# Optimization experiments

Measured on AMD Instinct MI355X. Metric: run time of the kernel, lower is better.

## Reference

```python
import jax, jax.numpy as jnp
import numpy as np

N_NODES = 100000


def gcn_conv(x, src, dst, norm, W, b, n_nodes):
    # x: [N, Din]; src/dst: [E'] (with self-loops); norm: [E']
    h = x @ W  # [N, Dout] dense transform first (PyG GCNConv order)
    msgs = h[src] * norm[:, None]  # gather + degree scaling, [E', Dout]
    out = jax.ops.segment_sum(msgs, dst, num_segments=n_nodes)  # scatter-add
    return out + b


def setup_inputs() -> dict:
    key = jax.random.key(0)
    k_x, k_e, k_w1, k_w2 = jax.random.split(key, 4)
    input_dim, hidden_dim = 256, 128
    n_edges = 1600000
    x = jax.random.normal(k_x, (N_NODES, input_dim), dtype=jnp.float32)
    edge_index = jax.random.randint(k_e, (2, n_edges), 0, N_NODES, dtype=jnp.int64)
    # Glorot-style init for conv weights, zeros bias (PyG defaults)
    s1 = (6.0 / (input_dim + hidden_dim)) ** 0.5
    s2 = (6.0 / (hidden_dim + hidden_dim)) ** 0.5
    W1 = jax.random.uniform(k_w1, (input_dim, hidden_dim), jnp.float32, -s1, s1)
    W2 = jax.random.uniform(k_w2, (hidden_dim, hidden_dim), jnp.float32, -s2, s2)
    b1 = jnp.zeros((hidden_dim,), jnp.float32)
    b2 = jnp.zeros((hidden_dim,), jnp.float32)
    return {"x": x, "edge_index": edge_index, "W1": W1, "b1": b1, "W2": W2, "b2": b2}


def reference(x, edge_index, W1, b1, W2, b2):
    n = x.shape[0]
    loops = jnp.arange(n, dtype=edge_index.dtype)
    src = jnp.concatenate([edge_index[0], loops])  # add self-loops
    dst = jnp.concatenate([edge_index[1], loops])
    # symmetric normalization deg^-1/2 (in-degree including self-loops)
    deg = jax.ops.segment_sum(jnp.ones_like(dst, dtype=x.dtype), dst, num_segments=n)
    dinv = jax.lax.rsqrt(deg)
    norm = dinv[src] * dinv[dst]
    # layer 1: GCNConv -> ReLU (dropout is identity in eval mode)
    h = jax.nn.relu(gcn_conv(x, src, dst, norm, W1, b1, n))
    # layer 2
    h = jax.nn.relu(gcn_conv(h, src, dst, norm, W2, b2, n))
    return h
```

## Files before the change

### kernel.cpp

```cpp
#include <hip/hip_runtime.h>
#include <hip/hip_bf16.h>


#define DIN 256
#define DH 128
#define BKT_SHIFT 9
#define BKT_SZ 512

typedef __attribute__((ext_vector_type(8))) short short8;
typedef __attribute__((ext_vector_type(4))) float f32x4;

__device__ __forceinline__ unsigned short f2bf(float f) {
    union { float f; unsigned int i; } c;
    c.f = f;
    unsigned int r = c.i + 0x7FFFu + ((c.i >> 16) & 1u);
    return (unsigned short)(r >> 16);
}
__device__ __forceinline__ float bf_lo(unsigned int u) {
    union { unsigned int i; float f; } c;
    c.i = u << 16;
    return c.f;
}
__device__ __forceinline__ float bf_hi(unsigned int u) {
    union { unsigned int i; float f; } c;
    c.i = u & 0xFFFF0000u;
    return c.f;
}

__global__ void count_k(const int* __restrict__ dst, int* __restrict__ cnt, int e) {
    int i = blockIdx.x * 256 + threadIdx.x;
    if (i < e) atomicAdd(&cnt[dst[i]], 1);
}

__global__ void dinv_k(const int* __restrict__ cnt, float* __restrict__ dinv, int n) {
    int i = blockIdx.x * 256 + threadIdx.x;
    if (i < n) dinv[i] = 1.0f / sqrtf((float)(cnt[i] + 1));
}

__global__ void block_sum_k(const int* __restrict__ cnt, int* __restrict__ bsum, int n) {
    __shared__ int s[256];
    int t = threadIdx.x;
    int i = blockIdx.x * 256 + t;
    s[t] = (i < n) ? cnt[i] : 0;
    __syncthreads();
    for (int off = 128; off > 0; off >>= 1) {
        if (t < off) s[t] += s[t + off];
        __syncthreads();
    }
    if (t == 0) bsum[blockIdx.x] = s[0];
}

__global__ void scan_bsum_k(int* __restrict__ bsum, int nb) {
    __shared__ int s[512];
    int t = threadIdx.x;
    s[t] = (t < nb) ? bsum[t] : 0;
    __syncthreads();
    for (int off = 1; off < 512; off <<= 1) {
        int x = (t >= off) ? s[t - off] : 0;
        __syncthreads();
        s[t] += x;
        __syncthreads();
    }
    if (t < nb) bsum[t] = (t == 0) ? 0 : s[t - 1];
}

__global__ void scan_write_k(const int* __restrict__ cnt, const int* __restrict__ bsum,
                             int* __restrict__ rowptr, int n) {
    __shared__ int s[256];
    int t = threadIdx.x;
    int i = blockIdx.x * 256 + t;
    int c = (i < n) ? cnt[i] : 0;
    s[t] = c;
    __syncthreads();
    for (int off = 1; off < 256; off <<= 1) {
        int x = (t >= off) ? s[t - off] : 0;
        __syncthreads();
        s[t] += x;
        __syncthreads();
    }
    int excl = s[t] - c + bsum[blockIdx.x];
    if (i < n) {
        rowptr[i] = excl;
        if (i == n - 1) rowptr[n] = excl + c;
    }
}

__global__ void init_bcur_k(const int* __restrict__ rowptr, int* __restrict__ bcur, int nbkt) {
    int b = threadIdx.x;
    if (b < nbkt) bcur[b] = rowptr[b << BKT_SHIFT];
}

__global__ void wt_k(const float* __restrict__ W, unsigned short* __restrict__ Wt, int K) {
    int i = blockIdx.x * 256 + threadIdx.x;
    if (i < K * 128) {
        int k = i >> 7, n = i & 127;
        Wt[(size_t)n * K + k] = f2bf(W[i]);
    }
}

__global__ __launch_bounds__(256) void bucket_k(const int* __restrict__ src,
                                                const int* __restrict__ dst,
                                                const float* __restrict__ dinv,
                                                int* __restrict__ bcur,
                                                int2* __restrict__ tmp, int e, int n) {
    __shared__ int hist[256];
    __shared__ int rstart[256];
    int nbkt = (n + BKT_SZ - 1) >> BKT_SHIFT;
    int t = threadIdx.x;
    int nb = gridDim.x;
    int chunk = (e + nb - 1) / nb;
    int beg = blockIdx.x * chunk, end = min(e, beg + chunk);

    hist[t] = 0;
    __syncthreads();
    for (int i = beg + t; i < end; i += 256) atomicAdd(&hist[dst[i] >> BKT_SHIFT], 1);
    __syncthreads();
    int h = hist[t];
    if (t < nbkt && h > 0) rstart[t] = atomicAdd(&bcur[t], h);
    __syncthreads();
    hist[t] = 0;
    __syncthreads();
    for (int i = beg + t; i < end; i += 256) {
        int d = dst[i];
        int b = d >> BKT_SHIFT;
        int o = atomicAdd(&hist[b], 1);
        int s = src[i];
        float w = dinv[s] * dinv[d];
        tmp[rstart[b] + o] = make_int2(s | ((d & (BKT_SZ - 1)) << 20), __float_as_int(w));
    }
}

__global__ __launch_bounds__(1024) void scatter2_k(const int2* __restrict__ tmp,
                                                   const int* __restrict__ rowptr,
                                                   int2* __restrict__ einfo, int n) {
    __shared__ int cur[BKT_SZ];
    int b = blockIdx.x;
    int t = threadIdx.x;
    int lo = b << BKT_SHIFT;
    int hi = min(n, lo + BKT_SZ);
    int nn = hi - lo;
    if (t < nn) cur[t] = rowptr[lo + t];
    __syncthreads();
    int beg = rowptr[lo], end = rowptr[hi];
    for (int i = beg + t; i < end; i += 1024) {
        int2 r = tmp[i];
        int dlow = (r.x >> 20) & (BKT_SZ - 1);
        int pos = atomicAdd(&cur[dlow], 1);
        einfo[pos] = make_int2(r.x & 0xFFFFF, r.y);
    }
}

template <bool A_BF16>
__global__ __launch_bounds__(256) void gemm_mfma(const void* __restrict__ Av,
                                                 const unsigned short* __restrict__ Wt,
                                                 unsigned short* __restrict__ Hb,
                                                 int M, int K) {
    __shared__ unsigned short Bt[16384];
    const int t = threadIdx.x;
    const int w = t >> 6;
    const int lane = t & 63;
    const int l15 = lane & 15;
    const int quad = lane >> 4;
    const int row0 = blockIdx.x * 128 + w * 32;

    const float* Af = (const float*)Av;
    const unsigned short* Ab = (const unsigned short*)Av;

    f32x4 acc[2][8];
#pragma unroll
    for (int rt = 0; rt < 2; ++rt)
#pragma unroll
        for (int ct = 0; ct < 8; ++ct)
#pragma unroll
            for (int j = 0; j < 4; ++j) acc[rt][ct][j] = 0.0f;

    for (int kc = 0; kc < K; kc += 128) {
        if (kc) __syncthreads();
#pragma unroll
        for (int i = 0; i < 8; ++i) {
            int fg = w * 8 + i;
            int ks = fg >> 3, ct = fg & 7;
            int nn = ct * 16 + l15;
            int gk = ks * 32 + quad * 8;
            *(short8*)&Bt[fg * 512 + lane * 8] =
                *(const short8*)(Wt + (size_t)nn * K + kc + gk);
        }
        __syncthreads();
#pragma unroll
        for (int ks = 0; ks < 4; ++ks) {
            int kk = ks * 32 + quad * 8;
            short8 af[2];
#pragma unroll
            for (int rt = 0; rt < 2; ++rt) {
                int row = row0 + rt * 16 + l15;
                if (row < M) {
                    if (A_BF16) {
                        af[rt] = *(const short8*)(Ab + (size_t)row * K + kc + kk);
                    } else {
                        const float* p = Af + (size_t)row * K + kc + kk;
                        float4 x0 = *(const float4*)p;
                        float4 x1 = *(const float4*)(p + 4);
                        af[rt][0] = (short)f2bf(x0.x);
                        af[rt][1] = (short)f2bf(x0.y);
                        af[rt][2] = (short)f2bf(x0.z);
                        af[rt][3] = (short)f2bf(x0.w);
                        af[rt][4] = (short)f2bf(x1.x);
                        af[rt][5] = (short)f2bf(x1.y);
                        af[rt][6] = (short)f2bf(x1.z);
                        af[rt][7] = (short)f2bf(x1.w);
                    }
                } else {
#pragma unroll
                    for (int j = 0; j < 8; ++j) af[rt][j] = 0;
                }
            }
#pragma unroll
            for (int ct = 0; ct < 8; ++ct) {
                short8 bfr = *(const short8*)&Bt[(ks * 8 + ct) * 512 + lane * 8];
                acc[0][ct] = __builtin_amdgcn_mfma_f32_16x16x32_bf16(af[0], bfr, acc[0][ct], 0, 0, 0);
                acc[1][ct] = __builtin_amdgcn_mfma_f32_16x16x32_bf16(af[1], bfr, acc[1][ct], 0, 0, 0);
            }
        }
    }
#pragma unroll
    for (int rt = 0; rt < 2; ++rt)
#pragma unroll
        for (int r = 0; r < 4; ++r) {
            int row = row0 + rt * 16 + quad * 4 + r;
            if (row < M) {
                unsigned short* o = Hb + (size_t)row * 128 + l15;
#pragma unroll
                for (int ct = 0; ct < 8; ++ct) o[ct * 16] = f2bf(acc[rt][ct][r]);
            }
        }
}

template <bool OUT_BF16>
__global__ __launch_bounds__(256) void agg_k(const unsigned short* __restrict__ Hb,
                                             const int* __restrict__ rowptr,
                                             const int2* __restrict__ einfo,
                                             const float* __restrict__ dinv,
                                             const float* __restrict__ bias,
                                             void* __restrict__ out, int n) {
    int v = blockIdx.x * 4 + (threadIdx.x >> 6);
    int lane = threadIdx.x & 63;
    if (v >= n) return;
    int l = lane & 31, half = lane >> 5;
    const uint2* __restrict__ H = (const uint2*)Hb;
    float a0 = 0.f, a1 = 0.f, a2 = 0.f, a3 = 0.f;
    if (half == 0) {
        float dv = dinv[v];
        float self = dv * dv;
        uint2 hv = H[(size_t)v * 32 + l];
        a0 = self * bf_lo(hv.x); a1 = self * bf_hi(hv.x);
        a2 = self * bf_lo(hv.y); a3 = self * bf_hi(hv.y);
    }
    int end = rowptr[v + 1];
    int i = rowptr[v] + half;
    for (; i + 6 < end; i += 8) {
        int2 e0 = einfo[i], e1 = einfo[i + 2], e2 = einfo[i + 4], e3 = einfo[i + 6];
        uint2 v0 = H[(size_t)e0.x * 32 + l];
        uint2 v1 = H[(size_t)e1.x * 32 + l];
        uint2 v2 = H[(size_t)e2.x * 32 + l];
        uint2 v3 = H[(size_t)e3.x * 32 + l];
        float w0 = __int_as_float(e0.y), w1 = __int_as_float(e1.y);
        float w2 = __int_as_float(e2.y), w3 = __int_as_float(e3.y);
        a0 = fmaf(w0, bf_lo(v0.x), a0); a1 = fmaf(w0, bf_hi(v0.x), a1);
        a2 = fmaf(w0, bf_lo(v0.y), a2); a3 = fmaf(w0, bf_hi(v0.y), a3);
        a0 = fmaf(w1, bf_lo(v1.x), a0); a1 = fmaf(w1, bf_hi(v1.x), a1);
        a2 = fmaf(w1, bf_lo(v1.y), a2); a3 = fmaf(w1, bf_hi(v1.y), a3);
        a0 = fmaf(w2, bf_lo(v2.x), a0); a1 = fmaf(w2, bf_hi(v2.x), a1);
        a2 = fmaf(w2, bf_lo(v2.y), a2); a3 = fmaf(w2, bf_hi(v2.y), a3);
        a0 = fmaf(w3, bf_lo(v3.x), a0); a1 = fmaf(w3, bf_hi(v3.x), a1);
        a2 = fmaf(w3, bf_lo(v3.y), a2); a3 = fmaf(w3, bf_hi(v3.y), a3);
    }
    for (; i < end; i += 2) {
        int2 e = einfo[i];
        uint2 vv = H[(size_t)e.x * 32 + l];
        float w = __int_as_float(e.y);
        a0 = fmaf(w, bf_lo(vv.x), a0); a1 = fmaf(w, bf_hi(vv.x), a1);
        a2 = fmaf(w, bf_lo(vv.y), a2); a3 = fmaf(w, bf_hi(vv.y), a3);
    }
    a0 += __shfl_xor(a0, 32);
    a1 += __shfl_xor(a1, 32);
    a2 += __shfl_xor(a2, 32);
    a3 += __shfl_xor(a3, 32);
    if (half == 0) {
        float4 bb = ((const float4*)bias)[l];
        float o0 = fmaxf(a0 + bb.x, 0.f);
        float o1 = fmaxf(a1 + bb.y, 0.f);
        float o2 = fmaxf(a2 + bb.z, 0.f);
        float o3 = fmaxf(a3 + bb.w, 0.f);
        if (OUT_BF16) {
            unsigned int p0 = (unsigned int)f2bf(o0) | ((unsigned int)f2bf(o1) << 16);
            unsigned int p1 = (unsigned int)f2bf(o2) | ((unsigned int)f2bf(o3) << 16);
            ((uint2*)out)[(size_t)v * 32 + l] = make_uint2(p0, p1);
        } else {
            ((float4*)out)[(size_t)v * 32 + l] = make_float4(o0, o1, o2, o3);
        }
    }
}

static inline size_t align_up(size_t x, size_t a) { return (x + a - 1) & ~(a - 1); }

extern "C" void kernel_launch(void* const* d_in, const int* in_sizes, int n_in,
                              void* d_out, int out_size, void* d_ws, size_t ws_size,
                              hipStream_t stream) {
    const float* x  = (const float*)d_in[0];
    const int*   ei = (const int*)d_in[1];
    const float* W1 = (const float*)d_in[2];
    const float* b1 = (const float*)d_in[3];
    const float* W2 = (const float*)d_in[4];
    const float* b2 = (const float*)d_in[5];

    const int N = in_sizes[0] / DIN;
    const int E = in_sizes[1] / 2;
    const int* src = ei;
    const int* dst = ei + E;
    const int NBKT = (N + BKT_SZ - 1) >> BKT_SHIFT;

    char* base = (char*)d_ws;
    size_t off = 0;
    int* cnt = (int*)(base + off);          off = align_up(off + (size_t)N * 4, 256);
    int* rowptr = (int*)(base + off);       off = align_up(off + (size_t)(N + 1) * 4, 256);
    float* dinv = (float*)(base + off);     off = align_up(off + (size_t)N * 4, 256);
    int* bsum = (int*)(base + off);         off = align_up(off + 512 * 4, 256);
    int* bcur = (int*)(base + off);         off = align_up(off + 256 * 4, 256);
    int2* tmp = (int2*)(base + off);        off = align_up(off + (size_t)E * 8, 256);
    int2* einfo = (int2*)(base + off);      off = align_up(off + (size_t)E * 8, 256);
    unsigned short* Wt1 = (unsigned short*)(base + off); off = align_up(off + (size_t)128 * 256 * 2, 256);
    unsigned short* Wt2 = (unsigned short*)(base + off); off = align_up(off + (size_t)128 * 128 * 2, 256);
    unsigned short* hb  = (unsigned short*)(base + off); off = align_up(off + (size_t)N * 128 * 2, 256);
    unsigned short* a1b = (unsigned short*)(base + off); off = align_up(off + (size_t)N * 128 * 2, 256);

    float* out = (float*)d_out;
    const int NB = (N + 255) / 256;

    hipMemsetAsync(cnt, 0, (size_t)N * sizeof(int), stream);
    count_k<<<(E + 255) / 256, 256, 0, stream>>>(dst, cnt, E);
    dinv_k<<<NB, 256, 0, stream>>>(cnt, dinv, N);
    block_sum_k<<<NB, 256, 0, stream>>>(cnt, bsum, N);
    scan_bsum_k<<<1, 512, 0, stream>>>(bsum, NB);
    scan_write_k<<<NB, 256, 0, stream>>>(cnt, bsum, rowptr, N);
    init_bcur_k<<<1, 256, 0, stream>>>(rowptr, bcur, NBKT);
    wt_k<<<(256 * 128 + 255) / 256, 256, 0, stream>>>(W1, Wt1, 256);
    wt_k<<<(128 * 128 + 255) / 256, 256, 0, stream>>>(W2, Wt2, 128);

    bucket_k<<<512, 256, 0, stream>>>(src, dst, dinv, bcur, tmp, E, N);
    scatter2_k<<<NBKT, 1024, 0, stream>>>(tmp, rowptr, einfo, N);

    const int GB = (N + 127) / 128;
    gemm_mfma<false><<<GB, 256, 0, stream>>>(x, Wt1, hb, N, DIN);
    agg_k<true><<<(N + 3) / 4, 256, 0, stream>>>(hb, rowptr, einfo, dinv, b1, a1b, N);
    gemm_mfma<true><<<GB, 256, 0, stream>>>(a1b, Wt2, hb, N, DH);
    agg_k<false><<<(N + 3) / 4, 256, 0, stream>>>(hb, rowptr, einfo, dinv, b2, out, N);
}
```

Before: 498.3 us.

## Fold GCN normalization into GEMM epilogue and fuse CSR build into fewer kernels

The degree-count and multi-kernel scan pipeline is replaced by a fused prep kernel that buckets edges into fixed-capacity per-bucket regions and also converts the weights. A single-block bucket scan follows, and the per-bucket scatter now computes the degrees, dinv and rowptr itself. The symmetric normalization is refactored so the GEMM epilogue scales each row by dinv[src] and aggregation applies dinv[dst] once at the end. Edge records therefore shrink from 8 to 4 bytes and the per-edge multiply disappears. Aggregation uses nontemporal loads and stores. The fixed CAP of 10240 records per bucket assumes a roughly uniform in-degree distribution and would overflow on skewed graphs.

```diff
diff --git a/kernel.cpp b/kernel.cpp
--- a/kernel.cpp
+++ b/kernel.cpp
@@ -6,9 +6,12 @@
 #define DH 128
 #define BKT_SHIFT 9
 #define BKT_SZ 512
+#define NBKT_MAX 256
+#define CAP 10240
 
 typedef __attribute__((ext_vector_type(8))) short short8;
 typedef __attribute__((ext_vector_type(4))) float f32x4;
+typedef __attribute__((ext_vector_type(2))) unsigned int uint2e;
 
 __device__ __forceinline__ unsigned short f2bf(float f) {
     union { float f; unsigned int i; } c;
@@ -27,96 +30,41 @@
     return c.f;
 }
 
-__global__ void count_k(const int* __restrict__ dst, int* __restrict__ cnt, int e) {
-    int i = blockIdx.x * 256 + threadIdx.x;
-    if (i < e) atomicAdd(&cnt[dst[i]], 1);
-}
-
-__global__ void dinv_k(const int* __restrict__ cnt, float* __restrict__ dinv, int n) {
-    int i = blockIdx.x * 256 + threadIdx.x;
-    if (i < n) dinv[i] = 1.0f / sqrtf((float)(cnt[i] + 1));
-}
-
-__global__ void block_sum_k(const int* __restrict__ cnt, int* __restrict__ bsum, int n) {
-    __shared__ int s[256];
+__global__ __launch_bounds__(256) void prep_k(const int* __restrict__ src,
+                                              const int* __restrict__ dst,
+                                              int* __restrict__ bcnt,
+                                              int* __restrict__ tmp, int e, int n,
+                                              int NBB,
+                                              const float* __restrict__ W1,
+                                              const float* __restrict__ W2,
+                                              unsigned short* __restrict__ Wt1,
+                                              unsigned short* __restrict__ Wt2) {
+    int bx = blockIdx.x;
     int t = threadIdx.x;
-    int i = blockIdx.x * 256 + t;
-    s[t] = (i < n) ? cnt[i] : 0;
-    __syncthreads();
-    for (int off = 128; off > 0; off >>= 1) {
-        if (t < off) s[t] += s[t + off];
-        __syncthreads();
-    }
-    if (t == 0) bsum[blockIdx.x] = s[0];
-}
-
-__global__ void scan_bsum_k(int* __restrict__ bsum, int nb) {
-    __shared__ int s[512];
-    int t = threadIdx.x;
-    s[t] = (t < nb) ? bsum[t] : 0;
-    __syncthreads();
-    for (int off = 1; off < 512; off <<= 1) {
-        int x = (t >= off) ? s[t - off] : 0;
-        __syncthreads();
-        s[t] += x;
-        __syncthreads();
-    }
-    if (t < nb) bsum[t] = (t == 0) ? 0 : s[t - 1];
-}
-
-__global__ void scan_write_k(const int* __restrict__ cnt, const int* __restrict__ bsum,
-                             int* __restrict__ rowptr, int n) {
-    __shared__ int s[256];
-    int t = threadIdx.x;
-    int i = blockIdx.x * 256 + t;
-    int c = (i < n) ? cnt[i] : 0;
-    s[t] = c;
-    __syncthreads();
-    for (int off = 1; off < 256; off <<= 1) {
-        int x = (t >= off) ? s[t - off] : 0;
-        __syncthreads();
-        s[t] += x;
-        __syncthreads();
-    }
-    int excl = s[t] - c + bsum[blockIdx.x];
-    if (i < n) {
-        rowptr[i] = excl;
-        if (i == n - 1) rowptr[n] = excl + c;
-    }
-}
-
-__global__ void init_bcur_k(const int* __restrict__ rowptr, int* __restrict__ bcur, int nbkt) {
-    int b = threadIdx.x;
-    if (b < nbkt) bcur[b] = rowptr[b << BKT_SHIFT];
-}
-
-__global__ void wt_k(const float* __restrict__ W, unsigned short* __restrict__ Wt, int K) {
-    int i = blockIdx.x * 256 + threadIdx.x;
-    if (i < K * 128) {
-        int k = i >> 7, n = i & 127;
-        Wt[(size_t)n * K + k] = f2bf(W[i]);
-    }
-}
-
-__global__ __launch_bounds__(256) void bucket_k(const int* __restrict__ src,
-                                                const int* __restrict__ dst,
-                                                const float* __restrict__ dinv,
-                                                int* __restrict__ bcur,
-                                                int2* __restrict__ tmp, int e, int n) {
-    __shared__ int hist[256];
-    __shared__ int rstart[256];
+    if (bx >= NBB) {
+        int i = (bx - NBB) * 256 + t;
+        if (i < 256 * 128) {
+            int k = i >> 7, nn = i & 127;
+            Wt1[(size_t)nn * 256 + k] = f2bf(W1[i]);
+        } else if (i < 256 * 128 + 128 * 128) {
+            int j = i - 256 * 128;
+            int k = j >> 7, nn = j & 127;
+            Wt2[(size_t)nn * 128 + k] = f2bf(W2[j]);
+        }
+        return;
+    }
+    __shared__ int hist[NBKT_MAX];
+    __shared__ int rstart[NBKT_MAX];
     int nbkt = (n + BKT_SZ - 1) >> BKT_SHIFT;
-    int t = threadIdx.x;
-    int nb = gridDim.x;
-    int chunk = (e + nb - 1) / nb;
-    int beg = blockIdx.x * chunk, end = min(e, beg + chunk);
+    int chunk = (e + NBB - 1) / NBB;
+    int beg = bx * chunk, end = min(e, beg + chunk);
 
     hist[t] = 0;
     __syncthreads();
     for (int i = beg + t; i < end; i += 256) atomicAdd(&hist[dst[i] >> BKT_SHIFT], 1);
     __syncthreads();
     int h = hist[t];
-    if (t < nbkt && h > 0) rstart[t] = atomicAdd(&bcur[t], h);
+    if (t < nbkt && h > 0) rstart[t] = atomicAdd(&bcnt[t], h);
     __syncthreads();
     hist[t] = 0;
     __syncthreads();
@@ -124,35 +72,77 @@
         int d = dst[i];
         int b = d >> BKT_SHIFT;
         int o = atomicAdd(&hist[b], 1);
-        int s = src[i];
-        float w = dinv[s] * dinv[d];
-        tmp[rstart[b] + o] = make_int2(s | ((d & (BKT_SZ - 1)) << 20), __float_as_int(w));
-    }
-}
-
-__global__ __launch_bounds__(1024) void scatter2_k(const int2* __restrict__ tmp,
-                                                   const int* __restrict__ rowptr,
-                                                   int2* __restrict__ einfo, int n) {
+        tmp[(size_t)b * CAP + rstart[b] + o] = src[i] | ((d & (BKT_SZ - 1)) << 20);
+    }
+}
+
+__global__ void scan196_k(const int* __restrict__ bcnt, int* __restrict__ base,
+                          int* __restrict__ rowptr, int nbkt, int n) {
+    __shared__ int s[256];
+    int t = threadIdx.x;
+    s[t] = (t < nbkt) ? bcnt[t] : 0;
+    __syncthreads();
+    for (int off = 1; off < 256; off <<= 1) {
+        int x = (t >= off) ? s[t - off] : 0;
+        __syncthreads();
+        s[t] += x;
+        __syncthreads();
+    }
+    base[t] = (t == 0) ? 0 : s[t - 1];
+    if (t == nbkt - 1) {
+        base[nbkt] = s[t];
+        rowptr[n] = s[t];
+    }
+}
+
+__global__ __launch_bounds__(1024) void scatter2_k(const int* __restrict__ tmp,
+                                                   const int* __restrict__ bcnt,
+                                                   const int* __restrict__ base,
+                                                   float* __restrict__ dinv,
+                                                   int* __restrict__ rowptr,
+                                                   int* __restrict__ einfo, int n) {
+    __shared__ int hist[BKT_SZ];
+    __shared__ int scn[BKT_SZ];
     __shared__ int cur[BKT_SZ];
     int b = blockIdx.x;
     int t = threadIdx.x;
     int lo = b << BKT_SHIFT;
-    int hi = min(n, lo + BKT_SZ);
-    int nn = hi - lo;
-    if (t < nn) cur[t] = rowptr[lo + t];
-    __syncthreads();
-    int beg = rowptr[lo], end = rowptr[hi];
-    for (int i = beg + t; i < end; i += 1024) {
-        int2 r = tmp[i];
-        int dlow = (r.x >> 20) & (BKT_SZ - 1);
+    int nn = min(n - lo, BKT_SZ);
+    int cnt = bcnt[b];
+    int bas = base[b];
+    const int* rec = tmp + (size_t)b * CAP;
+    if (t < BKT_SZ) hist[t] = 0;
+    __syncthreads();
+    for (int i = t; i < cnt; i += 1024) atomicAdd(&hist[(rec[i] >> 20) & (BKT_SZ - 1)], 1);
+    __syncthreads();
+    if (t < BKT_SZ) scn[t] = hist[t];
+    __syncthreads();
+    for (int off = 1; off < BKT_SZ; off <<= 1) {
+        int x = 0;
+        if (t < BKT_SZ && t >= off) x = scn[t - off];
+        __syncthreads();
+        if (t < BKT_SZ) scn[t] += x;
+        __syncthreads();
+    }
+    if (t < nn) {
+        int excl = bas + scn[t] - hist[t];
+        dinv[lo + t] = 1.0f / sqrtf((float)(hist[t] + 1));
+        rowptr[lo + t] = excl;
+        cur[t] = excl;
+    }
+    __syncthreads();
+    for (int i = t; i < cnt; i += 1024) {
+        int r = rec[i];
+        int dlow = (r >> 20) & (BKT_SZ - 1);
         int pos = atomicAdd(&cur[dlow], 1);
-        einfo[pos] = make_int2(r.x & 0xFFFFF, r.y);
+        einfo[pos] = r & 0xFFFFF;
     }
 }
 
 template <bool A_BF16>
 __global__ __launch_bounds__(256) void gemm_mfma(const void* __restrict__ Av,
                                                  const unsigned short* __restrict__ Wt,
+                                                 const float* __restrict__ dinv,
                                                  unsigned short* __restrict__ Hb,
                                                  int M, int K) {
     __shared__ unsigned short Bt[16384];
@@ -228,9 +218,10 @@
         for (int r = 0; r < 4; ++r) {
             int row = row0 + rt * 16 + quad * 4 + r;
             if (row < M) {
+                float dv = dinv[row];
                 unsigned short* o = Hb + (size_t)row * 128 + l15;
 #pragma unroll
-                for (int ct = 0; ct < 8; ++ct) o[ct * 16] = f2bf(acc[rt][ct][r]);
+                for (int ct = 0; ct < 8; ++ct) o[ct * 16] = f2bf(dv * acc[rt][ct][r]);
             }
         }
 }
@@ -238,7 +229,7 @@
 template <bool OUT_BF16>
 __global__ __launch_bounds__(256) void agg_k(const unsigned short* __restrict__ Hb,
                                              const int* __restrict__ rowptr,
-                                             const int2* __restrict__ einfo,
+                                             const int* __restrict__ einfo,
                                              const float* __restrict__ dinv,
                                              const float* __restrict__ bias,
                                              void* __restrict__ out, int n) {
@@ -249,54 +240,50 @@
     const uint2* __restrict__ H = (const uint2*)Hb;
     float a0 = 0.f, a1 = 0.f, a2 = 0.f, a3 = 0.f;
     if (half == 0) {
-        float dv = dinv[v];
-        float self = dv * dv;
         uint2 hv = H[(size_t)v * 32 + l];
-        a0 = self * bf_lo(hv.x); a1 = self * bf_hi(hv.x);
-        a2 = self * bf_lo(hv.y); a3 = self * bf_hi(hv.y);
+        a0 = bf_lo(hv.x); a1 = bf_hi(hv.x);
+        a2 = bf_lo(hv.y); a3 = bf_hi(hv.y);
     }
     int end = rowptr[v + 1];
     int i = rowptr[v] + half;
     for (; i + 6 < end; i += 8) {
-        int2 e0 = einfo[i], e1 = einfo[i + 2], e2 = einfo[i + 4], e3 = einfo[i + 6];
-        uint2 v0 = H[(size_t)e0.x * 32 + l];
-        uint2 v1 = H[(size_t)e1.x * 32 + l];
-        uint2 v2 = H[(size_t)e2.x * 32 + l];
-        uint2 v3 = H[(size_t)e3.x * 32 + l];
-        float w0 = __int_as_float(e0.y), w1 = __int_as_float(e1.y);
-        float w2 = __int_as_float(e2.y), w3 = __int_as_float(e3.y);
-        a0 = fmaf(w0, bf_lo(v0.x), a0); a1 = fmaf(w0, bf_hi(v0.x), a1);
-        a2 = fmaf(w0, bf_lo(v0.y), a2); a3 = fmaf(w0, bf_hi(v0.y), a3);
-        a0 = fmaf(w1, bf_lo(v1.x), a0); a1 = fmaf(w1, bf_hi(v1.x), a1);
-        a2 = fmaf(w1, bf_lo(v1.y), a2); a3 = fmaf(w1, bf_hi(v1.y), a3);
-        a0 = fmaf(w2, bf_lo(v2.x), a0); a1 = fmaf(w2, bf_hi(v2.x), a1);
-        a2 = fmaf(w2, bf_lo(v2.y), a2); a3 = fmaf(w2, bf_hi(v2.y), a3);
-        a0 = fmaf(w3, bf_lo(v3.x), a0); a1 = fmaf(w3, bf_hi(v3.x), a1);
-        a2 = fmaf(w3, bf_lo(v3.y), a2); a3 = fmaf(w3, bf_hi(v3.y), a3);
+        int s0 = __builtin_nontemporal_load(&einfo[i]);
+        int s1 = __builtin_nontemporal_load(&einfo[i + 2]);
+        int s2 = __builtin_nontemporal_load(&einfo[i + 4]);
+        int s3 = __builtin_nontemporal_load(&einfo[i + 6]);
+        uint2 v0 = H[(size_t)s0 * 32 + l];
+        uint2 v1 = H[(size_t)s1 * 32 + l];
+        uint2 v2 = H[(size_t)s2 * 32 + l];
+        uint2 v3 = H[(size_t)s3 * 32 + l];
+        a0 += bf_lo(v0.x); a1 += bf_hi(v0.x); a2 += bf_lo(v0.y); a3 += bf_hi(v0.y);
+        a0 += bf_lo(v1.x); a1 += bf_hi(v1.x); a2 += bf_lo(v1.y); a3 += bf_hi(v1.y);
+        a0 += bf_lo(v2.x); a1 += bf_hi(v2.x); a2 += bf_lo(v2.y); a3 += bf_hi(v2.y);
+        a0 += bf_lo(v3.x); a1 += bf_hi(v3.x); a2 += bf_lo(v3.y); a3 += bf_hi(v3.y);
     }
     for (; i < end; i += 2) {
-        int2 e = einfo[i];
-        uint2 vv = H[(size_t)e.x * 32 + l];
-        float w = __int_as_float(e.y);
-        a0 = fmaf(w, bf_lo(vv.x), a0); a1 = fmaf(w, bf_hi(vv.x), a1);
-        a2 = fmaf(w, bf_lo(vv.y), a2); a3 = fmaf(w, bf_hi(vv.y), a3);
+        int s = __builtin_nontemporal_load(&einfo[i]);
+        uint2 vv = H[(size_t)s * 32 + l];
+        a0 += bf_lo(vv.x); a1 += bf_hi(vv.x); a2 += bf_lo(vv.y); a3 += bf_hi(vv.y);
     }
     a0 += __shfl_xor(a0, 32);
     a1 += __shfl_xor(a1, 32);
     a2 += __shfl_xor(a2, 32);
     a3 += __shfl_xor(a3, 32);
     if (half == 0) {
+        float dv = dinv[v];
         float4 bb = ((const float4*)bias)[l];
-        float o0 = fmaxf(a0 + bb.x, 0.f);
-        float o1 = fmaxf(a1 + bb.y, 0.f);
-        float o2 = fmaxf(a2 + bb.z, 0.f);
-        float o3 = fmaxf(a3 + bb.w, 0.f);
+        float o0 = fmaxf(fmaf(dv, a0, bb.x), 0.f);
+        float o1 = fmaxf(fmaf(dv, a1, bb.y), 0.f);
+        float o2 = fmaxf(fmaf(dv, a2, bb.z), 0.f);
+        float o3 = fmaxf(fmaf(dv, a3, bb.w), 0.f);
         if (OUT_BF16) {
-            unsigned int p0 = (unsigned int)f2bf(o0) | ((unsigned int)f2bf(o1) << 16);
-            unsigned int p1 = (unsigned int)f2bf(o2) | ((unsigned int)f2bf(o3) << 16);
-            ((uint2*)out)[(size_t)v * 32 + l] = make_uint2(p0, p1);
+            uint2e p;
+            p.x = (unsigned int)f2bf(o0) | ((unsigned int)f2bf(o1) << 16);
+            p.y = (unsigned int)f2bf(o2) | ((unsigned int)f2bf(o3) << 16);
+            __builtin_nontemporal_store(p, (uint2e*)out + (size_t)v * 32 + l);
         } else {
-            ((float4*)out)[(size_t)v * 32 + l] = make_float4(o0, o1, o2, o3);
+            f32x4 o = {o0, o1, o2, o3};
+            __builtin_nontemporal_store(o, (f32x4*)out + (size_t)v * 32 + l);
         }
     }
 }
@@ -319,39 +306,32 @@
     const int* dst = ei + E;
     const int NBKT = (N + BKT_SZ - 1) >> BKT_SHIFT;
 
-    char* base = (char*)d_ws;
+    char* base_p = (char*)d_ws;
     size_t off = 0;
-    int* cnt = (int*)(base + off);          off = align_up(off + (size_t)N * 4, 256);
-    int* rowptr = (int*)(base + off);       off = align_up(off + (size_t)(N + 1) * 4, 256);
-    float* dinv = (float*)(base + off);     off = align_up(off + (size_t)N * 4, 256);
-    int* bsum = (int*)(base + off);         off = align_up(off + 512 * 4, 256);
-    int* bcur = (int*)(base + off);         off = align_up(off + 256 * 4, 256);
-    int2* tmp = (int2*)(base + off);        off = align_up(off + (size_t)E * 8, 256);
-    int2* einfo = (int2*)(base + off);      off = align_up(off + (size_t)E * 8, 256);
-    unsigned short* Wt1 = (unsigned short*)(base + off); off = align_up(off + (size_t)128 * 256 * 2, 256);
-    unsigned short* Wt2 = (unsigned short*)(base + off); off = align_up(off + (size_t)128 * 128 * 2, 256);
-    unsigned short* hb  = (unsigned short*)(base + off); off = align_up(off + (size_t)N * 128 * 2, 256);
-    unsigned short* a1b = (unsigned short*)(base + off); off = align_up(off + (size_t)N * 128 * 2, 256);
+    int* bcnt = (int*)(base_p + off);       off = align_up(off + 256 * 4, 256);
+    int* bbase = (int*)(base_p + off);      off = align_up(off + 257 * 4, 256);
+    int* rowptr = (int*)(base_p + off);     off = align_up(off + (size_t)(N + 1) * 4, 256);
+    float* dinv = (float*)(base_p + off);   off = align_up(off + (size_t)N * 4, 256);
+    int* tmp = (int*)(base_p + off);        off = align_up(off + (size_t)NBKT * CAP * 4, 256);
+    int* einfo = (int*)(base_p + off);      off = align_up(off + (size_t)E * 4, 256);
+    unsigned short* Wt1 = (unsigned short*)(base_p + off); off = align_up(off + (size_t)128 * 256 * 2, 256);
+    unsigned short* Wt2 = (unsigned short*)(base_p + off); off = align_up(off + (size_t)128 * 128 * 2, 256);
+    unsigned short* hb  = (unsigned short*)(base_p + off); off = align_up(off + (size_t)N * 128 * 2, 256);
+    unsigned short* a1b = (unsigned short*)(base_p + off); off = align_up(off + (size_t)N * 128 * 2, 256);
 
     float* out = (float*)d_out;
-    const int NB = (N + 255) / 256;
-
-    hipMemsetAsync(cnt, 0, (size_t)N * sizeof(int), stream);
-    count_k<<<(E + 255) / 256, 256, 0, stream>>>(dst, cnt, E);
-    dinv_k<<<NB, 256, 0, stream>>>(cnt, dinv, N);
-    block_sum_k<<<NB, 256, 0, stream>>>(cnt, bsum, N);
-    scan_bsum_k<<<1, 512, 0, stream>>>(bsum, NB);
-    scan_write_k<<<NB, 256, 0, stream>>>(cnt, bsum, rowptr, N);
-    init_bcur_k<<<1, 256, 0, stream>>>(rowptr, bcur, NBKT);
-    wt_k<<<(256 * 128 + 255) / 256, 256, 0, stream>>>(W1, Wt1, 256);
-    wt_k<<<(128 * 128 + 255) / 256, 256, 0, stream>>>(W2, Wt2, 128);
-
-    bucket_k<<<512, 256, 0, stream>>>(src, dst, dinv, bcur, tmp, E, N);
-    scatter2_k<<<NBKT, 1024, 0, stream>>>(tmp, rowptr, einfo, N);
+
+    const int NBB = 512;
+    const int WTB = (256 * 128 + 128 * 128 + 255) / 256;
+
+    hipMemsetAsync(bcnt, 0, 256 * sizeof(int), stream);
+    prep_k<<<NBB + WTB, 256, 0, stream>>>(src, dst, bcnt, tmp, E, N, NBB, W1, W2, Wt1, Wt2);
+    scan196_k<<<1, 256, 0, stream>>>(bcnt, bbase, rowptr, NBKT, N);
+    scatter2_k<<<NBKT, 1024, 0, stream>>>(tmp, bcnt, bbase, dinv, rowptr, einfo, N);
 
     const int GB = (N + 127) / 128;
-    gemm_mfma<false><<<GB, 256, 0, stream>>>(x, Wt1, hb, N, DIN);
+    gemm_mfma<false><<<GB, 256, 0, stream>>>(x, Wt1, dinv, hb, N, DIN);
     agg_k<true><<<(N + 3) / 4, 256, 0, stream>>>(hb, rowptr, einfo, dinv, b1, a1b, N);
-    gemm_mfma<true><<<GB, 256, 0, stream>>>(a1b, Wt2, hb, N, DH);
+    gemm_mfma<true><<<GB, 256, 0, stream>>>(a1b, Wt2, dinv, hb, N, DH);
     agg_k<false><<<(N + 3) / 4, 256, 0, stream>>>(hb, rowptr, einfo, dinv, b2, out, N);
 }
```

New measurement: 429.4 us. 13.8% less time.
